# Kernel tuning notes

Measured on AMD Instinct MI355X. Metric: run time of the kernel, lower is better.

## Reference

```python
import jax, jax.numpy as jnp
import numpy as np

INPUT_DIM = 1024
OUTPUT_DIM = 512
N_QUBITS = 12
DEPTH = 8
BATCH = 32768
LN_EPS = 1e-5
NOISE = 0.01


def setup_inputs() -> dict:
    key = jax.random.key(0)
    ks = jax.random.split(key, 12)
    inp = {
        "x": jax.random.normal(ks[0], (BATCH, INPUT_DIM), dtype=jnp.float32),
        "w_in": jax.random.normal(ks[1], (N_QUBITS, INPUT_DIM), dtype=jnp.float32) * 0.03,
        "b_in": jnp.zeros((N_QUBITS,), jnp.float32),
        "ln_g": jnp.ones((N_QUBITS,), jnp.float32),
        "ln_b": jnp.zeros((N_QUBITS,), jnp.float32),
        "rot": jax.random.normal(ks[2], (DEPTH, N_QUBITS, 3), dtype=jnp.float32) * 0.1,
        "ent": jax.random.normal(ks[3], (DEPTH, N_QUBITS - 1), dtype=jnp.float32) * 0.1,
        "w1": jax.random.normal(ks[4], (N_QUBITS, N_QUBITS), dtype=jnp.float32) * 0.3,
        "b1": jnp.zeros((N_QUBITS,), jnp.float32),
        "w2": jax.random.normal(ks[5], (OUTPUT_DIM, N_QUBITS), dtype=jnp.float32) * 0.3,
        "b2": jnp.zeros((OUTPUT_DIM,), jnp.float32),
        "meas_basis": jax.random.normal(ks[6], (N_QUBITS,), dtype=jnp.float32) * 0.1,
    }
    return inp


def _entangle(state, c):
    # c: sigmoid(ent[layer]) shape [n-1]. Effective (traced) torch semantics:
    # out[i]   = s[i]*(1-c_i)   + s[i+1]*c_i     for i in 0..n-2
    # out[n-1] = s[n-1]*(1-c_{n-2}) + s[n-2]*c_{n-2}
    left = state[:, :-1] * (1.0 - c) + state[:, 1:] * c          # [B, n-1]
    last = state[:, -1] * (1.0 - c[-1]) + state[:, -2] * c[-1]   # [B]
    return jnp.concatenate([left, last[:, None]], axis=1)


def reference(x, w_in, b_in, ln_g, ln_b, rot, ent, w1, b1, w2, b2, meas_basis):
    # input layer + layernorm + tanh
    h = x @ w_in.T + b_in                                   # [B, n]
    mu = jnp.mean(h, axis=-1, keepdims=True)
    var = jnp.mean((h - mu) ** 2, axis=-1, keepdims=True)
    h = (h - mu) * jax.lax.rsqrt(var + LN_EPS) * ln_g + ln_b
    h = jnp.tanh(h)

    encoded = h * jnp.float32(np.pi)
    state = jnp.zeros_like(encoded)
    for layer in range(DEPTH):
        rx = encoded + rot[layer, :, 0]
        state = state * jnp.cos(rx * 0.5) + jnp.sin(rot[layer, :, 1] * 0.5)
        state = state * jnp.cos(rot[layer, :, 2] * 0.5)     # Re(exp(i*rz/2))
        if layer < DEPTH - 1:
            state = _entangle(state, jax.nn.sigmoid(ent[layer]))

    # measurement: basis rotation + gaussian noise + tanh
    measured = state * jnp.tanh(meas_basis)
    noise = jax.random.normal(jax.random.key(1234), measured.shape, dtype=measured.dtype) * NOISE
    measured = jnp.tanh(measured + noise)

    # output MLP
    out = jax.nn.relu(measured @ w1.T + b1) @ w2.T + b2     # [B, OUTPUT_DIM]
    return out
```

## Files before the change

### kernel.cpp

```cpp
#include <hip/hip_runtime.h>
#include <cstdint>
#include <cstddef>


__device__ __forceinline__ uint32_t rotl32(uint32_t x, int r) {
  return (x << r) | (x >> (32 - r));
}

__device__ __forceinline__ void threefry2x32(uint32_t k0, uint32_t k1,
                                             uint32_t& x0, uint32_t& x1) {
  const uint32_t k2 = k0 ^ k1 ^ 0x1BD11BDAu;
  x0 += k0; x1 += k1;
#define TF_R(r) { x0 += x1; x1 = rotl32(x1, (r)); x1 ^= x0; }
  TF_R(13) TF_R(15) TF_R(26) TF_R(6)
  x0 += k1; x1 += k2 + 1u;
  TF_R(17) TF_R(29) TF_R(16) TF_R(24)
  x0 += k2; x1 += k0 + 2u;
  TF_R(13) TF_R(15) TF_R(26) TF_R(6)
  x0 += k0; x1 += k1 + 3u;
  TF_R(17) TF_R(29) TF_R(16) TF_R(24)
  x0 += k1; x1 += k2 + 4u;
  TF_R(13) TF_R(15) TF_R(26) TF_R(6)
  x0 += k2; x1 += k0 + 5u;
#undef TF_R
}

__device__ __forceinline__ float erfinv_xla(float x) {
  float w = -log1pf(-x * x);
  float p;
  if (w < 5.0f) {
    w -= 2.5f;
    p = 2.81022636e-08f;
    p = fmaf(p, w, 3.43273939e-07f);
    p = fmaf(p, w, -3.5233877e-06f);
    p = fmaf(p, w, -4.39150654e-06f);
    p = fmaf(p, w, 0.00021858087f);
    p = fmaf(p, w, -0.00125372503f);
    p = fmaf(p, w, -0.00417768164f);
    p = fmaf(p, w, 0.246640727f);
    p = fmaf(p, w, 1.50140941f);
  } else {
    w = sqrtf(w) - 3.0f;
    p = -0.000200214257f;
    p = fmaf(p, w, 0.000100950558f);
    p = fmaf(p, w, 0.00134934322f);
    p = fmaf(p, w, -0.00367342844f);
    p = fmaf(p, w, 0.00573950773f);
    p = fmaf(p, w, -0.0076224613f);
    p = fmaf(p, w, 0.00943887047f);
    p = fmaf(p, w, 1.00167406f);
    p = fmaf(p, w, 2.83297682f);
  }
  return p * x;
}

__global__ __launch_bounds__(256, 2)
void qnn_gemm_in(const float* __restrict__ x, const float* __restrict__ w_in,
                 const float* __restrict__ b_in, float* __restrict__ h) {
  __shared__ float wl[12 * 1024];
  {
    const float4* ws = (const float4*)w_in;
    float4* wd = (float4*)wl;
#pragma unroll
    for (int j = 0; j < 12; ++j) wd[threadIdx.x + 256 * j] = ws[threadIdx.x + 256 * j];
  }
  __syncthreads();

  const int wave = threadIdx.x >> 6;
  const int lane = threadIdx.x & 63;
  const float bmy = (lane < 12) ? b_in[lane] : 0.0f;

#pragma unroll
  for (int blk = 0; blk < 2; ++blk) {
    const int row0 = (blockIdx.x << 5) + (wave << 3) + (blk << 2);

    float4 xv[4][4];
#pragma unroll
    for (int r = 0; r < 4; ++r) {
      const float4* xr = (const float4*)(x + (size_t)(row0 + r) * 1024);
#pragma unroll
      for (int ks = 0; ks < 4; ++ks) xv[r][ks] = xr[(ks << 6) + lane];
    }

    float acc[4][12];
#pragma unroll
    for (int r = 0; r < 4; ++r)
#pragma unroll
      for (int q = 0; q < 12; ++q) acc[r][q] = 0.0f;

#pragma unroll
    for (int q = 0; q < 12; ++q) {
#pragma unroll
      for (int ks = 0; ks < 4; ++ks) {
        const float4 wv = *(const float4*)&wl[q * 1024 + (ks << 8) + (lane << 2)];
#pragma unroll
        for (int r = 0; r < 4; ++r) {
          acc[r][q] = fmaf(xv[r][ks].x, wv.x,
                      fmaf(xv[r][ks].y, wv.y,
                      fmaf(xv[r][ks].z, wv.z,
                      fmaf(xv[r][ks].w, wv.w, acc[r][q]))));
        }
      }
    }

#pragma unroll
    for (int r = 0; r < 4; ++r) {
      float hv[12];
#pragma unroll
      for (int q = 0; q < 12; ++q) {
        float v = acc[r][q];
        v += __shfl_xor(v, 1);
        v += __shfl_xor(v, 2);
        v += __shfl_xor(v, 4);
        v += __shfl_xor(v, 8);
        v += __shfl_xor(v, 16);
        v += __shfl_xor(v, 32);
        hv[q] = v;
      }
      float outv = hv[0];
#pragma unroll
      for (int q = 1; q < 12; ++q) outv = (lane == q) ? hv[q] : outv;
      if (lane < 12) h[(size_t)(row0 + r) * 12 + lane] = outv + bmy;
    }
  }
}

__global__ __launch_bounds__(256, 4)
void qnn_tail(const float* __restrict__ h_in,
              const float* __restrict__ ln_g, const float* __restrict__ ln_b,
              const float* __restrict__ rot,  const float* __restrict__ ent,
              const float* __restrict__ w1,   const float* __restrict__ b1,
              const float* __restrict__ w2,   const float* __restrict__ b2,
              const float* __restrict__ meas, float* __restrict__ out) {
  __shared__ float w2s[512 * 12];
  __shared__ float b2s[512];
  __shared__ float hid[32 * 12];
  __shared__ float rot0s[8 * 16], sr1s[8 * 16], cr2s[8 * 16], cens[8 * 16];
  __shared__ float tmbs[16], w1T[12 * 16], b1s[16], lgs[16], lbs[16];

  const int t = threadIdx.x;

  {
    const float4* s = (const float4*)w2;
    float4* d = (float4*)w2s;
#pragma unroll
    for (int j = 0; j < 6; ++j) d[t + 256 * j] = s[t + 256 * j];
    if (t < 128) ((float4*)b2s)[t] = ((const float4*)b2)[t];
    if (t < 96) {
      const int l = t / 12, q = t % 12, base = (l * 12 + q) * 3;
      rot0s[l * 16 + q] = rot[base + 0];
      sr1s[l * 16 + q]  = sinf(rot[base + 1] * 0.5f);
      cr2s[l * 16 + q]  = cosf(rot[base + 2] * 0.5f);
    }
    if (t >= 96 && t < 184) {
      const int i = t - 96, l = i / 11, q = i % 11;
      cens[l * 16 + q] = 1.0f / (1.0f + expf(-ent[l * 11 + q]));
    }
    if (t >= 184 && t < 196) tmbs[t - 184] = tanhf(meas[t - 184]);
    if (t >= 196 && t < 208) b1s[t - 196] = b1[t - 196];
    if (t >= 208 && t < 220) lgs[t - 208] = ln_g[t - 208];
    if (t >= 220 && t < 232) lbs[t - 220] = ln_b[t - 220];
    if (t < 144) { const int j = t / 12, q = t % 12; w1T[q * 16 + j] = w1[t]; }
  }
  __syncthreads();

  float wa[12], wb[12];
#pragma unroll
  for (int q = 0; q < 12; ++q) {
    wa[q] = w2s[t * 12 + q];
    wb[q] = w2s[(t + 256) * 12 + q];
  }
  const float ba = b2s[t], bb = b2s[t + 256];

  const int lane = t & 63;
  const int wv   = t >> 6;
  const int grp  = lane >> 4;
  const int q    = lane & 15;
  const int gb   = lane & 48;
  const bool act = (q < 12);
  const int cidx = (q == 11) ? 10 : q;

#pragma unroll
  for (int pass = 0; pass < 2; ++pass) {
    const int rl  = (pass << 4) + (wv << 2) + grp;
    const int row = (blockIdx.x << 5) + rl;

    float hq = act ? h_in[(size_t)row * 12 + q] : 0.0f;

    float s = hq;
    s += __shfl_xor(s, 1); s += __shfl_xor(s, 2);
    s += __shfl_xor(s, 4); s += __shfl_xor(s, 8);
    const float mu = s * (1.0f / 12.0f);
    float d = act ? (hq - mu) : 0.0f;
    float v2 = d * d;
    v2 += __shfl_xor(v2, 1); v2 += __shfl_xor(v2, 2);
    v2 += __shfl_xor(v2, 4); v2 += __shfl_xor(v2, 8);
    const float inv = 1.0f / sqrtf(v2 * (1.0f / 12.0f) + 1e-5f);

    const float n   = d * inv * lgs[q] + lbs[q];
    const float enc = tanhf(n) * 3.14159265358979f;

    float st = 0.0f;
#pragma unroll
    for (int l = 0; l < 8; ++l) {
      const float rx = enc + rot0s[l * 16 + q];
      st = st * cosf(rx * 0.5f) + sr1s[l * 16 + q];
      st *= cr2s[l * 16 + q];
      if (l < 7) {
        const float stn = __shfl(st, lane + 1);
        const float stp = __shfl(st, lane - 1);
        const float c   = cens[l * 16 + cidx];
        const float other = (q == 11) ? stp : stn;
        st = st * (1.0f - c) + other * c;
      }
    }

    uint32_t x0 = 0u, x1 = (uint32_t)row * 12u + (uint32_t)q;
    threefry2x32(0u, 1234u, x0, x1);
    const uint32_t bits = x0 ^ x1;
    const float u01 = __uint_as_float((bits >> 9) | 0x3F800000u) - 1.0f;
    float u = u01 * 2.0f + (-0.99999994f);
    u = fmaxf(-0.99999994f, u);
    const float nrm = 1.41421356237f * erfinv_xla(u);
    const float m = tanhf(st * tmbs[q] + nrm * 0.01f);

    float acc1 = b1s[q];
#pragma unroll
    for (int qq = 0; qq < 12; ++qq) {
      const float mq = __shfl(m, gb + qq);
      acc1 = fmaf(mq, w1T[qq * 16 + q], acc1);
    }
    if (act) hid[rl * 12 + q] = fmaxf(acc1, 0.0f);
  }
  __syncthreads();

  float* ob = out + (size_t)blockIdx.x * 32 * 512;
  for (int rr = 0; rr < 32; ++rr) {
    const float4 h0 = *(const float4*)&hid[rr * 12 + 0];
    const float4 h1 = *(const float4*)&hid[rr * 12 + 4];
    const float4 h2 = *(const float4*)&hid[rr * 12 + 8];
    const float hvv[12] = {h0.x, h0.y, h0.z, h0.w, h1.x, h1.y, h1.z, h1.w,
                           h2.x, h2.y, h2.z, h2.w};
    float a = ba, b = bb;
#pragma unroll
    for (int qq = 0; qq < 12; ++qq) {
      a = fmaf(hvv[qq], wa[qq], a);
      b = fmaf(hvv[qq], wb[qq], b);
    }
    ob[rr * 512 + t] = a;
    ob[rr * 512 + 256 + t] = b;
  }
}

extern "C" void kernel_launch(void* const* d_in, const int* in_sizes, int n_in,
                              void* d_out, int out_size, void* d_ws, size_t ws_size,
                              hipStream_t stream) {
  const float* x    = (const float*)d_in[0];
  const float* w_in = (const float*)d_in[1];
  const float* b_in = (const float*)d_in[2];
  const float* ln_g = (const float*)d_in[3];
  const float* ln_b = (const float*)d_in[4];
  const float* rot  = (const float*)d_in[5];
  const float* ent  = (const float*)d_in[6];
  const float* w1   = (const float*)d_in[7];
  const float* b1   = (const float*)d_in[8];
  const float* w2   = (const float*)d_in[9];
  const float* b2   = (const float*)d_in[10];
  const float* mb   = (const float*)d_in[11];
  float* outp = (float*)d_out;
  float* h    = (float*)d_ws;

  qnn_gemm_in<<<1024, 256, 0, stream>>>(x, w_in, b_in, h);
  qnn_tail<<<1024, 256, 0, stream>>>(h, ln_g, ln_b, rot, ent, w1, b1, w2, b2, mb, outp);
}
```

Baseline: 272.5 us.

## Restructure input GEMM with double-buffered LDS x tiles and per-row threads

Rewrites the input projection kernel so each block handles 64 rows. Tiles of x are staged through double-buffered shared memory while the next tile is being loaded, and each thread accumulates one row over a quarter of each K-slice. The weights are read directly from global memory as wave-uniform loads instead of being copied into a 48KB LDS buffer. This removes the per-row cross-lane shuffle reductions and the per-block weight copy, replacing them with a small LDS partial-sum reduction. The trade-off is more barriers, fewer blocks (512), and padded LDS rows that may still cause bank conflicts.

```diff
diff --git a/kernel.cpp b/kernel.cpp
--- a/kernel.cpp
+++ b/kernel.cpp
@@ -57,71 +57,83 @@
 __global__ __launch_bounds__(256, 2)
 void qnn_gemm_in(const float* __restrict__ x, const float* __restrict__ w_in,
                  const float* __restrict__ b_in, float* __restrict__ h) {
-  __shared__ float wl[12 * 1024];
-  {
-    const float4* ws = (const float4*)w_in;
-    float4* wd = (float4*)wl;
-#pragma unroll
-    for (int j = 0; j < 12; ++j) wd[threadIdx.x + 256 * j] = ws[threadIdx.x + 256 * j];
-  }
-  __syncthreads();
-
-  const int wave = threadIdx.x >> 6;
-  const int lane = threadIdx.x & 63;
-  const float bmy = (lane < 12) ? b_in[lane] : 0.0f;
-
-#pragma unroll
-  for (int blk = 0; blk < 2; ++blk) {
-    const int row0 = (blockIdx.x << 5) + (wave << 3) + (blk << 2);
-
-    float4 xv[4][4];
-#pragma unroll
-    for (int r = 0; r < 4; ++r) {
-      const float4* xr = (const float4*)(x + (size_t)(row0 + r) * 1024);
-#pragma unroll
-      for (int ks = 0; ks < 4; ++ks) xv[r][ks] = xr[(ks << 6) + lane];
-    }
-
-    float acc[4][12];
-#pragma unroll
-    for (int r = 0; r < 4; ++r)
-#pragma unroll
-      for (int q = 0; q < 12; ++q) acc[r][q] = 0.0f;
-
-#pragma unroll
-    for (int q = 0; q < 12; ++q) {
-#pragma unroll
-      for (int ks = 0; ks < 4; ++ks) {
-        const float4 wv = *(const float4*)&wl[q * 1024 + (ks << 8) + (lane << 2)];
-#pragma unroll
-        for (int r = 0; r < 4; ++r) {
-          acc[r][q] = fmaf(xv[r][ks].x, wv.x,
-                      fmaf(xv[r][ks].y, wv.y,
-                      fmaf(xv[r][ks].z, wv.z,
-                      fmaf(xv[r][ks].w, wv.w, acc[r][q]))));
-        }
+  __shared__ float xs[2][64][80];
+  __shared__ float ps[4][64][16];
+
+  const int tid  = threadIdx.x;
+  const int wave = tid >> 6;
+  const int lane = tid & 63;
+  const int rowg = blockIdx.x << 6;
+
+  const int brow = tid >> 4;
+  const int col4 = tid & 15;
+
+  float acc[12];
+#pragma unroll
+  for (int q = 0; q < 12; ++q) acc[q] = 0.0f;
+
+  float4 st0, st1, st2, st3;
+
+#define K1_STAGE_LOAD(T)                                                       \
+  {                                                                            \
+    const float* gb = x + (size_t)(rowg + brow) * 1024 + ((T) << 6) + (col4 << 2); \
+    st0 = *(const float4*)(gb);                                                \
+    st1 = *(const float4*)(gb + 16 * 1024);                                    \
+    st2 = *(const float4*)(gb + 32 * 1024);                                    \
+    st3 = *(const float4*)(gb + 48 * 1024);                                    \
+  }
+
+#define K1_STAGE_WRITE(BUF)                                                    \
+  {                                                                            \
+    *(float4*)&xs[BUF][brow +  0][col4 << 2] = st0;                            \
+    *(float4*)&xs[BUF][brow + 16][col4 << 2] = st1;                            \
+    *(float4*)&xs[BUF][brow + 32][col4 << 2] = st2;                            \
+    *(float4*)&xs[BUF][brow + 48][col4 << 2] = st3;                            \
+  }
+
+  K1_STAGE_LOAD(0)
+  K1_STAGE_WRITE(0)
+  __syncthreads();
+
+  for (int t = 0; t < 16; ++t) {
+    const int cur = t & 1;
+    if (t < 15) K1_STAGE_LOAD(t + 1)
+
+    const int kb = (t << 6) + (wave << 4);
+#pragma unroll
+    for (int kc = 0; kc < 4; ++kc) {
+      const float4 xv = *(const float4*)&xs[cur][lane][(wave << 4) + (kc << 2)];
+      const int kofs = kb + (kc << 2);
+#pragma unroll
+      for (int q = 0; q < 12; ++q) {
+        const float4 wv = *(const float4*)&w_in[q * 1024 + kofs];
+        acc[q] = fmaf(xv.x, wv.x,
+                 fmaf(xv.y, wv.y,
+                 fmaf(xv.z, wv.z,
+                 fmaf(xv.w, wv.w, acc[q]))));
       }
     }
 
-#pragma unroll
-    for (int r = 0; r < 4; ++r) {
-      float hv[12];
-#pragma unroll
-      for (int q = 0; q < 12; ++q) {
-        float v = acc[r][q];
-        v += __shfl_xor(v, 1);
-        v += __shfl_xor(v, 2);
-        v += __shfl_xor(v, 4);
-        v += __shfl_xor(v, 8);
-        v += __shfl_xor(v, 16);
-        v += __shfl_xor(v, 32);
-        hv[q] = v;
-      }
-      float outv = hv[0];
-#pragma unroll
-      for (int q = 1; q < 12; ++q) outv = (lane == q) ? hv[q] : outv;
-      if (lane < 12) h[(size_t)(row0 + r) * 12 + lane] = outv + bmy;
-    }
+    __syncthreads();
+    if (t < 15) {
+      K1_STAGE_WRITE(cur ^ 1)
+      __syncthreads();
+    }
+  }
+#undef K1_STAGE_LOAD
+#undef K1_STAGE_WRITE
+
+  *(float4*)&ps[wave][lane][0] = make_float4(acc[0], acc[1], acc[2], acc[3]);
+  *(float4*)&ps[wave][lane][4] = make_float4(acc[4], acc[5], acc[6], acc[7]);
+  *(float4*)&ps[wave][lane][8] = make_float4(acc[8], acc[9], acc[10], acc[11]);
+  __syncthreads();
+
+#pragma unroll
+  for (int i = 0; i < 3; ++i) {
+    const int o = tid + (i << 8);
+    const int row = o / 12, q = o - row * 12;
+    const float v = ps[0][row][q] + ps[1][row][q] + ps[2][row][q] + ps[3][row][q];
+    h[(size_t)(rowg + row) * 12 + q] = v + b_in[q];
   }
 }
 
@@ -270,6 +282,6 @@
   float* outp = (float*)d_out;
   float* h    = (float*)d_ws;
 
-  qnn_gemm_in<<<1024, 256, 0, stream>>>(x, w_in, b_in, h);
+  qnn_gemm_in<<<512, 256, 0, stream>>>(x, w_in, b_in, h);
   qnn_tail<<<1024, 256, 0, stream>>>(h, ln_g, ln_b, rot, ent, w1, b1, w2, b2, mb, outp);
 }
```

Measured after the change: 279.7 us. +2.7%, slower.
